# Optimization experiments

Measured on AMD Instinct MI355X. Metric: run time of the kernel, lower is better.

## Reference

```python
import jax, jax.numpy as jnp
import numpy as np

N, M, D = 65536, 8192, 3


def setup_inputs() -> dict:
    key = jax.random.key(0)
    k1, k2, k3 = jax.random.split(key, 3)
    input_vertex_set = jax.random.normal(k1, (N, D), dtype=jnp.float32)
    sampled_points = jax.random.normal(k2, (M, D), dtype=jnp.float32)
    probs = jax.random.uniform(k3, (M,), dtype=jnp.float32)
    return {
        "input_vertex_set": input_vertex_set,
        "sampled_points": sampled_points,
        "probs": probs,
    }


def reference(input_vertex_set, sampled_points, probs):
    x, y = input_vertex_set, sampled_points
    x2 = jnp.sum(x * x, axis=1)  # [N]
    y2 = jnp.sum(y * y, axis=1)  # [M]
    d2 = x2[:, None] + y2[None, :] - 2.0 * (x @ y.T)  # [N, M]
    d2 = jnp.maximum(d2, 0.0)  # guard tiny negatives from cancellation

    # l1: for each sampled point, distance to nearest input vertex, weighted by probs
    min_over_rows = jnp.min(d2, axis=0)  # [M]
    l1 = jnp.dot(probs, min_over_rows)

    # l2: for each input vertex, distance to nearest sampled point, weighted by
    # the prob of that nearest sampled point
    min_over_cols = jnp.min(d2, axis=1)   # [N]
    argmin_cols = jnp.argmin(d2, axis=1)  # [N] indices into M
    l2 = jnp.dot(jnp.take(probs, argmin_cols), min_over_cols)

    return l1 + l2
```

## Files before the change

### kernel.cpp

```cpp
#include <hip/hip_runtime.h>


constexpr int NP = 65536;
constexpr int MP = 8192;
constexpr int K = 32;
constexpr int KC = K * K * K;
constexpr float H = 0.265625f;
constexpr float R0 = 4.25f;

constexpr size_t OFF_CNT    = 0;
constexpr size_t OFF_FBCNT  = 262144;
constexpr size_t OFF_PART   = 262160;
constexpr size_t OFF_OFFS   = 524304;
constexpr size_t OFF_BSUM   = 786464;
constexpr size_t OFF_FBROW  = 787488;
constexpr size_t OFF_FBCOL  = 1049632;
constexpr size_t OFF_ROWKEY = 1082400;
constexpr size_t OFF_COLBIT = 1344544;
constexpr size_t OFF_PTS    = 1377312;

__device__ __forceinline__ int cellof(float v) {
    int c = (int)floorf((v + R0) * (1.0f / H));
    return min(max(c, 0), K - 1);
}
__device__ __forceinline__ unsigned umin32(unsigned a, unsigned b) { return a < b ? a : b; }

__global__ __launch_bounds__(256) void k_count(const float* __restrict__ x,
                                               const float* __restrict__ y,
                                               unsigned* __restrict__ cnt,
                                               unsigned* __restrict__ fbcnt) {
    int i = blockIdx.x * 256 + threadIdx.x;
    if (i == 0) { fbcnt[0] = 0; fbcnt[1] = 0; }
    if (i < NP) {
        int c = (cellof(x[3 * i + 2]) * K + cellof(x[3 * i + 1])) * K + cellof(x[3 * i]);
        atomicAdd(&cnt[c], 1u);
    } else if (i < NP + MP) {
        int j = i - NP;
        int c = (cellof(y[3 * j + 2]) * K + cellof(y[3 * j + 1])) * K + cellof(y[3 * j]);
        atomicAdd(&cnt[KC + c], 1u);
    }
}

template <bool WRITE_BSUM>
__device__ __forceinline__ void block_excl_scan(unsigned v, unsigned* dst, int g,
                                                unsigned* bsum) {
    int t = threadIdx.x;
    unsigned inc = v;
#pragma unroll
    for (int o = 1; o < 64; o <<= 1) {
        unsigned u = __shfl_up(inc, o, 64);
        if ((t & 63) >= o) inc += u;
    }
    __shared__ unsigned wtot[4];
    if ((t & 63) == 63) wtot[t >> 6] = inc;
    __syncthreads();
    unsigned woff = 0;
    for (int w = 0; w < (t >> 6); ++w) woff += wtot[w];
    dst[g] = woff + inc - v;
    if (WRITE_BSUM && t == 255) bsum[blockIdx.x] = woff + inc;
}

__global__ __launch_bounds__(256) void k_scan_a(const unsigned* __restrict__ cnt,
                                                unsigned* __restrict__ part,
                                                unsigned* __restrict__ bsum) {
    int g = blockIdx.x * 256 + threadIdx.x;
    block_excl_scan<true>(cnt[g], part, g, bsum);
}

__global__ __launch_bounds__(256) void k_scan_b(unsigned* __restrict__ bsum) {
    int t = threadIdx.x;
    block_excl_scan<false>(bsum[t], bsum, t, nullptr);
}

__global__ __launch_bounds__(256) void k_scan_c(const unsigned* __restrict__ cnt,
                                                unsigned* __restrict__ part,
                                                unsigned* __restrict__ offs,
                                                const unsigned* __restrict__ bsum) {
    int g = blockIdx.x * 256 + threadIdx.x;
    unsigned off = part[g] + bsum[blockIdx.x];
    offs[g] = off;
    part[g] = off;
    if (g == 2 * KC - 1) offs[2 * KC] = off + cnt[g];
}

__global__ __launch_bounds__(256) void k_scatter(const float* __restrict__ x,
                                                 const float* __restrict__ y,
                                                 unsigned* __restrict__ cursor,
                                                 float4* __restrict__ pts) {
    int i = blockIdx.x * 256 + threadIdx.x;
    if (i < NP) {
        float a = x[3 * i], b = x[3 * i + 1], c = x[3 * i + 2];
        int cc = (cellof(c) * K + cellof(b)) * K + cellof(a);
        unsigned s = atomicAdd(&cursor[cc], 1u);
        pts[s] = make_float4(a, b, c, __uint_as_float((unsigned)i));
    } else if (i < NP + MP) {
        int j = i - NP;
        float a = y[3 * j], b = y[3 * j + 1], c = y[3 * j + 2];
        int cc = (cellof(c) * K + cellof(b)) * K + cellof(a);
        unsigned s = atomicAdd(&cursor[KC + cc], 1u);
        pts[s] = make_float4(a, b, c, __uint_as_float((unsigned)j));
    }
}

template <int W, bool ROWS>
__device__ __forceinline__ void nn_body(int bid, const float4* __restrict__ pts,
                                        const unsigned* __restrict__ offs,
                                        unsigned* __restrict__ outv,
                                        unsigned* __restrict__ fbcnt,
                                        unsigned* __restrict__ fblist) {
    int t = threadIdx.x;
    int lane = t & (W - 1);
    int q = (bid * 256 + t) / W;
    float4 Q = pts[(ROWS ? 0 : NP) + q];
    unsigned qi = __float_as_uint(Q.w);
    int cx = cellof(Q.x), cy = cellof(Q.y), cz = cellof(Q.z);
    int x0c = max(cx - 1, 0), x1c = min(cx + 1, K - 1);
    int span = x1c - x0c + 1;
    constexpr int base = ROWS ? KC : 0;
    unsigned best = 0xFFFFFFFFu;
    for (int dz = -1; dz <= 1; ++dz) {
        int z = cz + dz;
        if (z < 0 || z >= K) continue;
        for (int dy = -1; dy <= 1; ++dy) {
            int yy = cy + dy;
            if (yy < 0 || yy >= K) continue;
            int cid = base + (z * K + yy) * K + x0c;
            unsigned s = offs[cid], e = offs[cid + span];
            for (unsigned j = s + lane; j < e; j += W) {
                float4 Pv = pts[j];
                float ddx = Q.x - Pv.x, ddy = Q.y - Pv.y, ddz = Q.z - Pv.z;
                float d2 = fmaf(ddx, ddx, fmaf(ddy, ddy, ddz * ddz));
                unsigned key = ROWS
                    ? ((__float_as_uint(d2) & 0xFFFFE000u) | __float_as_uint(Pv.w))
                    : __float_as_uint(d2);
                best = umin32(best, key);
            }
        }
    }
#pragma unroll
    for (int o = W / 2; o > 0; o >>= 1)
        best = umin32(best, (unsigned)__shfl_xor((int)best, o, 64));
    float lox = fmaf((float)cx, H, -R0);
    float loy = fmaf((float)cy, H, -R0);
    float loz = fmaf((float)cz, H, -R0);
    const float INF = __builtin_inff();
    float thr = INF;
    thr = fminf(thr, (cx == 0)     ? INF : Q.x - (lox - H));
    thr = fminf(thr, (cx == K - 1) ? INF : (lox + 2.f * H) - Q.x);
    thr = fminf(thr, (cy == 0)     ? INF : Q.y - (loy - H));
    thr = fminf(thr, (cy == K - 1) ? INF : (loy + 2.f * H) - Q.y);
    thr = fminf(thr, (cz == 0)     ? INF : Q.z - (loz - H));
    thr = fminf(thr, (cz == K - 1) ? INF : (loz + 2.f * H) - Q.z);
    float bd2 = __uint_as_float(ROWS ? (best & 0xFFFFE000u) : best);
    bool certified = (thr > 0.f) && (bd2 <= thr * thr);
    if (lane == 0) {
        outv[qi] = best;
        if (!certified) fblist[atomicAdd(&fbcnt[ROWS ? 0 : 1], 1u)] = qi;
    }
}

constexpr int RBLK = NP * 8 / 256;
constexpr int CBLK = MP * 16 / 256;

__global__ __launch_bounds__(256) void k_nn(const float4* __restrict__ pts,
                                            const unsigned* __restrict__ offs,
                                            unsigned* __restrict__ rowkey,
                                            unsigned* __restrict__ colbits,
                                            unsigned* __restrict__ fbcnt,
                                            unsigned* __restrict__ fbrow,
                                            unsigned* __restrict__ fbcol) {
    if (blockIdx.x < RBLK)
        nn_body<8, true>(blockIdx.x, pts, offs, rowkey, fbcnt, fbrow);
    else
        nn_body<16, false>(blockIdx.x - RBLK, pts, offs, colbits, fbcnt, fbcol);
}

constexpr int RSEG = 16, RSEGLEN = MP / RSEG;
constexpr int CSEG = 64, CSEGLEN = NP / CSEG;

__global__ __launch_bounds__(256) void k_fb(const float* __restrict__ x,
                                            const float* __restrict__ y,
                                            const float4* __restrict__ pts,
                                            const unsigned* __restrict__ fbcnt,
                                            const unsigned* __restrict__ fbrow,
                                            const unsigned* __restrict__ fbcol,
                                            unsigned* __restrict__ rowkey,
                                            unsigned* __restrict__ colbits) {
    int lane = threadIdx.x & 63;
    unsigned wid = (blockIdx.x * 256 + threadIdx.x) >> 6;
    unsigned nw = gridDim.x * 4;
    unsigned nr = fbcnt[0], nc = fbcnt[1];
    unsigned rtasks = nr * RSEG;
    for (unsigned tsk = wid; tsk < rtasks; tsk += nw) {
        unsigned q = tsk / RSEG, seg = tsk % RSEG;
        unsigned n = fbrow[q];
        float qx = x[3 * n], qy = x[3 * n + 1], qz = x[3 * n + 2];
        unsigned best = 0xFFFFFFFFu;
        int s0 = NP + seg * RSEGLEN;
#pragma unroll 2
        for (int s = s0 + lane; s < s0 + RSEGLEN; s += 64) {
            float4 Pv = pts[s];
            float ddx = qx - Pv.x, ddy = qy - Pv.y, ddz = qz - Pv.z;
            float d2 = fmaf(ddx, ddx, fmaf(ddy, ddy, ddz * ddz));
            best = umin32(best, (__float_as_uint(d2) & 0xFFFFE000u) | __float_as_uint(Pv.w));
        }
#pragma unroll
        for (int o = 32; o > 0; o >>= 1)
            best = umin32(best, (unsigned)__shfl_xor((int)best, o, 64));
        if (lane == 0) atomicMin(&rowkey[n], best);
    }
    unsigned ctasks = nc * CSEG;
    for (unsigned tsk = wid; tsk < ctasks; tsk += nw) {
        unsigned q = tsk / CSEG, seg = tsk % CSEG;
        unsigned m = fbcol[q];
        float qx = y[3 * m], qy = y[3 * m + 1], qz = y[3 * m + 2];
        unsigned bb = 0x7F800000u;
        int s0 = seg * CSEGLEN;
#pragma unroll 2
        for (int s = s0 + lane; s < s0 + CSEGLEN; s += 64) {
            float4 Pv = pts[s];
            float ddx = qx - Pv.x, ddy = qy - Pv.y, ddz = qz - Pv.z;
            float d2 = fmaf(ddx, ddx, fmaf(ddy, ddy, ddz * ddz));
            bb = umin32(bb, __float_as_uint(d2));
        }
#pragma unroll
        for (int o = 32; o > 0; o >>= 1)
            bb = umin32(bb, (unsigned)__shfl_xor((int)bb, o, 64));
        if (lane == 0) atomicMin(&colbits[m], bb);
    }
}

__global__ __launch_bounds__(256) void k3_reduce(const unsigned* __restrict__ rowkey,
                                                 const unsigned* __restrict__ colbits,
                                                 const float* __restrict__ probs,
                                                 float* __restrict__ out) {
    int i = blockIdx.x * 256 + threadIdx.x;
    float v = 0.f;
    if (i < NP) {
        unsigned k = rowkey[i];
        unsigned idx = k & 0x1FFFu;
        float dmin = __uint_as_float(k & 0xFFFFE000u);
        v = probs[idx] * dmin;
    } else {
        int m = i - NP;
        float dmin = __uint_as_float(colbits[m]);
        v = probs[m] * dmin;
    }
    for (int off = 32; off > 0; off >>= 1) v += __shfl_down(v, off, 64);
    __shared__ float wsum[4];
    int lane = threadIdx.x & 63;
    int w = threadIdx.x >> 6;
    if (lane == 0) wsum[w] = v;
    __syncthreads();
    if (threadIdx.x == 0) atomicAdd(out, wsum[0] + wsum[1] + wsum[2] + wsum[3]);
}

extern "C" void kernel_launch(void* const* d_in, const int* in_sizes, int n_in,
                              void* d_out, int out_size, void* d_ws, size_t ws_size,
                              hipStream_t stream) {
    const float* x = (const float*)d_in[0];
    const float* y = (const float*)d_in[1];
    const float* probs = (const float*)d_in[2];
    float* out = (float*)d_out;

    char* ws = (char*)d_ws;
    unsigned* cnt    = (unsigned*)(ws + OFF_CNT);
    unsigned* fbcnt  = (unsigned*)(ws + OFF_FBCNT);
    unsigned* part   = (unsigned*)(ws + OFF_PART);
    unsigned* offs   = (unsigned*)(ws + OFF_OFFS);
    unsigned* bsum   = (unsigned*)(ws + OFF_BSUM);
    unsigned* fbrow  = (unsigned*)(ws + OFF_FBROW);
    unsigned* fbcol  = (unsigned*)(ws + OFF_FBCOL);
    unsigned* rowkey = (unsigned*)(ws + OFF_ROWKEY);
    unsigned* colbits= (unsigned*)(ws + OFF_COLBIT);
    float4*   pts    = (float4*)(ws + OFF_PTS);

    hipMemsetAsync(cnt, 0, OFF_PART, stream);
    hipMemsetAsync(out, 0, sizeof(float), stream);

    constexpr int NB_PTS = (NP + MP) / 256;
    k_count<<<NB_PTS, 256, 0, stream>>>(x, y, cnt, fbcnt);
    k_scan_a<<<2 * KC / 256, 256, 0, stream>>>(cnt, part, bsum);
    k_scan_b<<<1, 256, 0, stream>>>(bsum);
    k_scan_c<<<2 * KC / 256, 256, 0, stream>>>(cnt, part, offs, bsum);
    k_scatter<<<NB_PTS, 256, 0, stream>>>(x, y, part, pts);
    k_nn<<<RBLK + CBLK, 256, 0, stream>>>(pts, offs, rowkey, colbits, fbcnt, fbrow, fbcol);
    k_fb<<<512, 256, 0, stream>>>(x, y, pts, fbcnt, fbrow, fbcol, rowkey, colbits);
    k3_reduce<<<NB_PTS, 256, 0, stream>>>(rowkey, colbits, probs, out);
}
```

Baseline: 112.7 us.

## Merge scan kernels into one block, hoist cell offsets, widen column lanes

Replaces the three-kernel prefix scan over cell counts with a single 1024-thread block in which each thread scans 64 counts using vectorized uint4 loads and writes both offsets and scatter cursors. Folds the output zeroing into k_count and drops one memset, cutting launch and dependency overhead. In the NN kernel, the nine row-range offset pairs are loaded up front so the loads are not serialized with the loops, and the column query group widens from 16 to 32 lanes. The single-block scan serializes 65536 counts on one CU, and wider column groups trade occupancy per query for more parallelism per cell.

```diff
diff --git a/kernel.cpp b/kernel.cpp
--- a/kernel.cpp
+++ b/kernel.cpp
@@ -28,9 +28,10 @@
 __global__ __launch_bounds__(256) void k_count(const float* __restrict__ x,
                                                const float* __restrict__ y,
                                                unsigned* __restrict__ cnt,
-                                               unsigned* __restrict__ fbcnt) {
+                                               unsigned* __restrict__ fbcnt,
+                                               float* __restrict__ out) {
     int i = blockIdx.x * 256 + threadIdx.x;
-    if (i == 0) { fbcnt[0] = 0; fbcnt[1] = 0; }
+    if (i == 0) { fbcnt[0] = 0; fbcnt[1] = 0; out[0] = 0.f; }
     if (i < NP) {
         int c = (cellof(x[3 * i + 2]) * K + cellof(x[3 * i + 1])) * K + cellof(x[3 * i]);
         atomicAdd(&cnt[c], 1u);
@@ -41,46 +42,43 @@
     }
 }
 
-template <bool WRITE_BSUM>
-__device__ __forceinline__ void block_excl_scan(unsigned v, unsigned* dst, int g,
-                                                unsigned* bsum) {
+__global__ __launch_bounds__(1024) void k_scan(const unsigned* __restrict__ cnt,
+                                               unsigned* __restrict__ offs,
+                                               unsigned* __restrict__ cursor) {
     int t = threadIdx.x;
-    unsigned inc = v;
+    const uint4* c4 = (const uint4*)cnt;
+    uint4 v[16];
+    unsigned sum = 0;
+#pragma unroll
+    for (int k = 0; k < 16; ++k) {
+        v[k] = c4[t * 16 + k];
+        sum += v[k].x + v[k].y + v[k].z + v[k].w;
+    }
+    unsigned inc = sum;
 #pragma unroll
     for (int o = 1; o < 64; o <<= 1) {
         unsigned u = __shfl_up(inc, o, 64);
         if ((t & 63) >= o) inc += u;
     }
-    __shared__ unsigned wtot[4];
-    if ((t & 63) == 63) wtot[t >> 6] = inc;
+    __shared__ unsigned wt[16];
+    if ((t & 63) == 63) wt[t >> 6] = inc;
     __syncthreads();
     unsigned woff = 0;
-    for (int w = 0; w < (t >> 6); ++w) woff += wtot[w];
-    dst[g] = woff + inc - v;
-    if (WRITE_BSUM && t == 255) bsum[blockIdx.x] = woff + inc;
-}
-
-__global__ __launch_bounds__(256) void k_scan_a(const unsigned* __restrict__ cnt,
-                                                unsigned* __restrict__ part,
-                                                unsigned* __restrict__ bsum) {
-    int g = blockIdx.x * 256 + threadIdx.x;
-    block_excl_scan<true>(cnt[g], part, g, bsum);
-}
-
-__global__ __launch_bounds__(256) void k_scan_b(unsigned* __restrict__ bsum) {
-    int t = threadIdx.x;
-    block_excl_scan<false>(bsum[t], bsum, t, nullptr);
-}
-
-__global__ __launch_bounds__(256) void k_scan_c(const unsigned* __restrict__ cnt,
-                                                unsigned* __restrict__ part,
-                                                unsigned* __restrict__ offs,
-                                                const unsigned* __restrict__ bsum) {
-    int g = blockIdx.x * 256 + threadIdx.x;
-    unsigned off = part[g] + bsum[blockIdx.x];
-    offs[g] = off;
-    part[g] = off;
-    if (g == 2 * KC - 1) offs[2 * KC] = off + cnt[g];
+    for (int w = 0; w < (t >> 6); ++w) woff += wt[w];
+    unsigned run = woff + inc - sum;
+    uint4* o4 = (uint4*)offs;
+    uint4* u4 = (uint4*)cursor;
+#pragma unroll
+    for (int k = 0; k < 16; ++k) {
+        uint4 w4;
+        w4.x = run; run += v[k].x;
+        w4.y = run; run += v[k].y;
+        w4.z = run; run += v[k].z;
+        w4.w = run; run += v[k].w;
+        o4[t * 16 + k] = w4;
+        u4[t * 16 + k] = w4;
+    }
+    if (t == 1023) offs[2 * KC] = run;
 }
 
 __global__ __launch_bounds__(256) void k_scatter(const float* __restrict__ x,
@@ -117,24 +115,30 @@
     int x0c = max(cx - 1, 0), x1c = min(cx + 1, K - 1);
     int span = x1c - x0c + 1;
     constexpr int base = ROWS ? KC : 0;
+    unsigned sb[9], eb[9];
+#pragma unroll
+    for (int r = 0; r < 9; ++r) {
+        int dz = r / 3 - 1, dy = r % 3 - 1;
+        int z = cz + dz, yy = cy + dy;
+        bool valid = (z >= 0) && (z < K) && (yy >= 0) && (yy < K);
+        int zc = min(max(z, 0), K - 1), yc = min(max(yy, 0), K - 1);
+        int cid = base + (zc * K + yc) * K + x0c;
+        unsigned s = offs[cid];
+        unsigned e = offs[cid + span];
+        sb[r] = valid ? s : 0;
+        eb[r] = valid ? e : 0;
+    }
     unsigned best = 0xFFFFFFFFu;
-    for (int dz = -1; dz <= 1; ++dz) {
-        int z = cz + dz;
-        if (z < 0 || z >= K) continue;
-        for (int dy = -1; dy <= 1; ++dy) {
-            int yy = cy + dy;
-            if (yy < 0 || yy >= K) continue;
-            int cid = base + (z * K + yy) * K + x0c;
-            unsigned s = offs[cid], e = offs[cid + span];
-            for (unsigned j = s + lane; j < e; j += W) {
-                float4 Pv = pts[j];
-                float ddx = Q.x - Pv.x, ddy = Q.y - Pv.y, ddz = Q.z - Pv.z;
-                float d2 = fmaf(ddx, ddx, fmaf(ddy, ddy, ddz * ddz));
-                unsigned key = ROWS
-                    ? ((__float_as_uint(d2) & 0xFFFFE000u) | __float_as_uint(Pv.w))
-                    : __float_as_uint(d2);
-                best = umin32(best, key);
-            }
+#pragma unroll
+    for (int r = 0; r < 9; ++r) {
+        for (unsigned j = sb[r] + lane; j < eb[r]; j += W) {
+            float4 Pv = pts[j];
+            float ddx = Q.x - Pv.x, ddy = Q.y - Pv.y, ddz = Q.z - Pv.z;
+            float d2 = fmaf(ddx, ddx, fmaf(ddy, ddy, ddz * ddz));
+            unsigned key = ROWS
+                ? ((__float_as_uint(d2) & 0xFFFFE000u) | __float_as_uint(Pv.w))
+                : __float_as_uint(d2);
+            best = umin32(best, key);
         }
     }
 #pragma unroll
@@ -160,7 +164,7 @@
 }
 
 constexpr int RBLK = NP * 8 / 256;
-constexpr int CBLK = MP * 16 / 256;
+constexpr int CBLK = MP * 32 / 256;
 
 __global__ __launch_bounds__(256) void k_nn(const float4* __restrict__ pts,
                                             const unsigned* __restrict__ offs,
@@ -172,7 +176,7 @@
     if (blockIdx.x < RBLK)
         nn_body<8, true>(blockIdx.x, pts, offs, rowkey, fbcnt, fbrow);
     else
-        nn_body<16, false>(blockIdx.x - RBLK, pts, offs, colbits, fbcnt, fbcol);
+        nn_body<32, false>(blockIdx.x - RBLK, pts, offs, colbits, fbcnt, fbcol);
 }
 
 constexpr int RSEG = 16, RSEGLEN = MP / RSEG;
@@ -266,24 +270,20 @@
     char* ws = (char*)d_ws;
     unsigned* cnt    = (unsigned*)(ws + OFF_CNT);
     unsigned* fbcnt  = (unsigned*)(ws + OFF_FBCNT);
-    unsigned* part   = (unsigned*)(ws + OFF_PART);
+    unsigned* cursor = (unsigned*)(ws + OFF_PART);
     unsigned* offs   = (unsigned*)(ws + OFF_OFFS);
-    unsigned* bsum   = (unsigned*)(ws + OFF_BSUM);
     unsigned* fbrow  = (unsigned*)(ws + OFF_FBROW);
     unsigned* fbcol  = (unsigned*)(ws + OFF_FBCOL);
     unsigned* rowkey = (unsigned*)(ws + OFF_ROWKEY);
     unsigned* colbits= (unsigned*)(ws + OFF_COLBIT);
     float4*   pts    = (float4*)(ws + OFF_PTS);
 
-    hipMemsetAsync(cnt, 0, OFF_PART, stream);
-    hipMemsetAsync(out, 0, sizeof(float), stream);
+    hipMemsetAsync(cnt, 0, 2 * KC * 4, stream);
 
     constexpr int NB_PTS = (NP + MP) / 256;
-    k_count<<<NB_PTS, 256, 0, stream>>>(x, y, cnt, fbcnt);
-    k_scan_a<<<2 * KC / 256, 256, 0, stream>>>(cnt, part, bsum);
-    k_scan_b<<<1, 256, 0, stream>>>(bsum);
-    k_scan_c<<<2 * KC / 256, 256, 0, stream>>>(cnt, part, offs, bsum);
-    k_scatter<<<NB_PTS, 256, 0, stream>>>(x, y, part, pts);
+    k_count<<<NB_PTS, 256, 0, stream>>>(x, y, cnt, fbcnt, out);
+    k_scan<<<1, 1024, 0, stream>>>(cnt, offs, cursor);
+    k_scatter<<<NB_PTS, 256, 0, stream>>>(x, y, cursor, pts);
     k_nn<<<RBLK + CBLK, 256, 0, stream>>>(pts, offs, rowkey, colbits, fbcnt, fbrow, fbcol);
     k_fb<<<512, 256, 0, stream>>>(x, y, pts, fbcnt, fbrow, fbcol, rowkey, colbits);
     k3_reduce<<<NB_PTS, 256, 0, stream>>>(rowkey, colbits, probs, out);
```

After: 117.8 us. +4.5%, slower.
